# Kernel optimization log

Hardware: AMD Instinct MI355X
Metric: run time of the kernel (lower is better)

Reference implementation:

```python
import jax, jax.numpy as jnp
import numpy as np

N_EMBD = 384
N_HEADS = 6
HEAD_SIZE = N_EMBD // N_HEADS  # 64
LN_EPS = 1e-5


def _layernorm(x, g, b):
    mu = jnp.mean(x, axis=-1, keepdims=True)
    var = jnp.var(x, axis=-1, keepdims=True)
    return (x - mu) * jax.lax.rsqrt(var + LN_EPS) * g + b


def setup_inputs() -> dict:
    key = jax.random.key(0)
    ks = jax.random.split(key, 12)
    B, T, C, H, D = 128, 256, N_EMBD, N_HEADS, HEAD_SIZE
    s_in = 1.0 / np.sqrt(C)
    s_ff = 1.0 / np.sqrt(4 * C)
    return {
        "x": jax.random.normal(ks[0], (B, T, C), dtype=jnp.float32),
        "ln1_g": jnp.ones((C,), jnp.float32),
        "ln1_b": jnp.zeros((C,), jnp.float32),
        "Wq": jax.random.uniform(ks[1], (H, C, D), jnp.float32, -s_in, s_in),
        "Wk": jax.random.uniform(ks[2], (H, C, D), jnp.float32, -s_in, s_in),
        "Wv": jax.random.uniform(ks[3], (H, C, D), jnp.float32, -s_in, s_in),
        "Wo": jax.random.uniform(ks[4], (C, C), jnp.float32, -s_in, s_in),
        "bo": jnp.zeros((C,), jnp.float32),
        "ln2_g": jnp.ones((C,), jnp.float32),
        "ln2_b": jnp.zeros((C,), jnp.float32),
        "W1": jax.random.uniform(ks[5], (C, 4 * C), jnp.float32, -s_in, s_in),
        "b1": jnp.zeros((4 * C,), jnp.float32),
        "W2": jax.random.uniform(ks[6], (4 * C, C), jnp.float32, -s_ff, s_ff),
        "b2": jnp.zeros((C,), jnp.float32),
    }


def reference(x, ln1_g, ln1_b, Wq, Wk, Wv, Wo, bo, ln2_g, ln2_b, W1, b1, W2, b2):
    # Dropout layers are identity (eval mode).
    B, T, C = x.shape
    h = _layernorm(x, ln1_g, ln1_b)
    # Per-head projections: [B,T,C] x [H,C,D] -> [B,H,T,D]
    q = jnp.einsum('btc,hcd->bhtd', h, Wq)
    k = jnp.einsum('btc,hcd->bhtd', h, Wk)
    v = jnp.einsum('btc,hcd->bhtd', h, Wv)
    scale = HEAD_SIZE ** (-0.5)
    scores = jnp.einsum('bhtd,bhsd->bhts', q, k) * scale  # [B,H,T,T]
    causal = jnp.tril(jnp.ones((T, T), dtype=bool))
    scores = jnp.where(causal, scores, jnp.float32(-jnp.inf))
    wei = jax.nn.softmax(scores, axis=-1)
    attn = jnp.einsum('bhts,bhsd->bhtd', wei, v)  # [B,H,T,D]
    attn = attn.transpose(0, 2, 1, 3).reshape(B, T, C)  # concat heads
    x = x + attn @ Wo + bo
    h2 = _layernorm(x, ln2_g, ln2_b)
    ff = jax.nn.relu(h2 @ W1 + b1) @ W2 + b2
    return x + ff
```

## Files before the change

kernel.cpp:

```cpp
#include <hip/hip_runtime.h>

typedef unsigned int u32;
typedef unsigned short u16;
typedef __bf16 bf16_t;
typedef float f32x4 __attribute__((ext_vector_type(4)));
typedef bf16_t bfrag __attribute__((ext_vector_type(8)));
typedef u16 u16x8 __attribute__((ext_vector_type(8)));
typedef u16 u16x4 __attribute__((ext_vector_type(4)));

__device__ inline u16 f2bf(float f) {
    union { float f; u32 u; } v; v.f = f;
    u32 r = v.u + 0x7fffu + ((v.u >> 16) & 1u);
    return (u16)(r >> 16);
}
__device__ inline float bf2f(u16 h) {
    union { u32 u; float f; } v; v.u = ((u32)h) << 16; return v.f;
}

__device__ inline f32x4 mfma16(bfrag a, bfrag b, f32x4 c) {
    return __builtin_amdgcn_mfma_f32_16x16x32_bf16(a, b, c, 0, 0, 0);
}

__device__ inline void gload_lds16(const void* g, void* l) {
    __builtin_amdgcn_global_load_lds((const __attribute__((address_space(1))) u32*)g,
                                     (__attribute__((address_space(3))) u32*)l, 16, 0, 0);
}

__device__ inline float redmax16(float v) {
    #pragma unroll
    for (int m = 1; m < 16; m <<= 1) v = fmaxf(v, __shfl_xor(v, m));
    return v;
}
__device__ inline float redsum16(float v) {
    #pragma unroll
    for (int m = 1; m < 16; m <<= 1) v += __shfl_xor(v, m);
    return v;
}

#define NTOK 32768
#define QKV_ELEMS 12582912

__global__ __launch_bounds__(256) void prep_weights(
    const float* __restrict__ Wq, const float* __restrict__ Wk,
    const float* __restrict__ Wv, const float* __restrict__ Wo,
    const float* __restrict__ W1, const float* __restrict__ W2,
    u16* __restrict__ wqkvT, u16* __restrict__ woT,
    u16* __restrict__ w1T, u16* __restrict__ w2T)
{
    __shared__ float tile[64][65];
    const int b = blockIdx.x;
    const float* src; u16* dst;
    int sr0, sc0, srs, dr0, dc0, drs;
    if (b < 36) {
        int i = b / 6, j = b - i * 6;
        src = Wo;  srs = 384;  sr0 = i * 64; sc0 = j * 64;
        dst = woT; drs = 384;  dr0 = j * 64; dc0 = i * 64;
    } else if (b < 180) {
        int t = b - 36; int i = t / 24, j = t - i * 24;
        src = W1;  srs = 1536; sr0 = i * 64; sc0 = j * 64;
        dst = w1T; drs = 384;  dr0 = j * 64; dc0 = i * 64;
    } else if (b < 324) {
        int t = b - 180; int i = t / 6, j = t - i * 6;
        src = W2;  srs = 384;  sr0 = i * 64; sc0 = j * 64;
        dst = w2T; drs = 1536; dr0 = j * 64; dc0 = i * 64;
    } else {
        int t = b - 324;
        int m2 = t / 36; t -= m2 * 36;
        int h = t / 6, tt = t - h * 6;
        src = (m2 == 0) ? Wq : ((m2 == 1) ? Wk : Wv);
        srs = 64;  sr0 = h * 384 + tt * 64; sc0 = 0;
        dst = wqkvT; drs = 384; dr0 = m2 * 384 + h * 64; dc0 = tt * 64;
    }
    const int lane = threadIdx.x & 63, grp = threadIdx.x >> 6;
    #pragma unroll
    for (int i = 0; i < 16; i++) {
        int r = grp * 16 + i;
        tile[r][lane] = src[(size_t)(sr0 + r) * srs + sc0 + lane];
    }
    __syncthreads();
    #pragma unroll
    for (int i = 0; i < 16; i++) {
        int r = grp * 16 + i;
        dst[(size_t)(dr0 + r) * drs + dc0 + lane] = f2bf(tile[lane][r]);
    }
}

__global__ __launch_bounds__(256) void ln_f32(
    const float* __restrict__ x, const float* __restrict__ g,
    const float* __restrict__ b, u16* __restrict__ out)
{
    const int row = blockIdx.x * 4 + (threadIdx.x >> 6);
    const int lane = threadIdx.x & 63;
    const float2* xr = (const float2*)(x + (size_t)row * 384);
    float2 v[3];
    float s = 0.f, s2 = 0.f;
    #pragma unroll
    for (int i = 0; i < 3; i++) {
        v[i] = xr[lane + i * 64];
        s += v[i].x + v[i].y; s2 += v[i].x * v[i].x + v[i].y * v[i].y;
    }
    #pragma unroll
    for (int m = 1; m < 64; m <<= 1) { s += __shfl_xor(s, m); s2 += __shfl_xor(s2, m); }
    float mean = s * (1.f / 384.f);
    float rstd = rsqrtf(s2 * (1.f / 384.f) - mean * mean + 1e-5f);
    u32* op = (u32*)(out + (size_t)row * 384);
    #pragma unroll
    for (int i = 0; i < 3; i++) {
        int c = (lane + i * 64) * 2;
        u32 lo = f2bf((v[i].x - mean) * rstd * g[c] + b[c]);
        u32 hi = f2bf((v[i].y - mean) * rstd * g[c + 1] + b[c + 1]);
        op[lane + i * 64] = lo | (hi << 16);
    }
}

__global__ __launch_bounds__(256) void ln_bf16(
    const u16* __restrict__ x, const float* __restrict__ g,
    const float* __restrict__ b, u16* __restrict__ out)
{
    const int row = blockIdx.x * 4 + (threadIdx.x >> 6);
    const int lane = threadIdx.x & 63;
    const u32* xr = (const u32*)(x + (size_t)row * 384);
    float vx[3], vy[3];
    float s = 0.f, s2 = 0.f;
    #pragma unroll
    for (int i = 0; i < 3; i++) {
        u32 w = xr[lane + i * 64];
        vx[i] = bf2f((u16)(w & 0xffffu));
        vy[i] = bf2f((u16)(w >> 16));
        s += vx[i] + vy[i]; s2 += vx[i] * vx[i] + vy[i] * vy[i];
    }
    #pragma unroll
    for (int m = 1; m < 64; m <<= 1) { s += __shfl_xor(s, m); s2 += __shfl_xor(s2, m); }
    float mean = s * (1.f / 384.f);
    float rstd = rsqrtf(s2 * (1.f / 384.f) - mean * mean + 1e-5f);
    u32* op = (u32*)(out + (size_t)row * 384);
    #pragma unroll
    for (int i = 0; i < 3; i++) {
        int c = (lane + i * 64) * 2;
        u32 lo = f2bf((vx[i] - mean) * rstd * g[c] + b[c]);
        u32 hi = f2bf((vy[i] - mean) * rstd * g[c + 1] + b[c + 1]);
        op[lane + i * 64] = lo | (hi << 16);
    }
}

template<int EPI, int NT>
__global__ __launch_bounds__(256, 4) void gemm_m97(
    const u16* __restrict__ A, const u16* __restrict__ Bt,
    const float* __restrict__ bias, const void* __restrict__ resid,
    void* __restrict__ outp, int M, int N)
{
    const int K = NT * 64;
    __shared__ __align__(16) u16 smem[17408];
    u16* As = smem;
    u16* Bs = smem + 8192;
    const int tid = threadIdx.x, wave = tid >> 6, lane = tid & 63;
    const int nbn = N >> 7;
    const int nwg = gridDim.x;
    const int bid = blockIdx.x;
    const int wg = (bid & 7) * (nwg >> 3) + (bid >> 3);
    const int bm = wg / nbn, bn = wg - bm * nbn;
    const int rowA0 = bm << 7, rowB0 = bn << 7;
    const int wm = (wave >> 1) << 6, wn = (wave & 1) << 6;
    const int lr = lane >> 3, lc = lane & 7;
    f32x4 acc[4][4] = {};

    for (int t = 0; t < NT; ++t) {
        const int ko = t << 6;
        #pragma unroll
        for (int p = 0; p < 4; p++) {
            const int idx = p * 4 + wave;
            const int r = idx * 8 + lr;
            const int csrc = ((lc ^ (r & 7)) << 3);
            gload_lds16(A + (size_t)(rowA0 + r) * K + ko + csrc, &As[idx * 512]);
            gload_lds16(Bt + (size_t)(rowB0 + r) * K + ko + csrc, &Bs[idx * 512]);
        }
        __syncthreads();
        #pragma unroll
        for (int kk = 0; kk < 2; kk++) {
            bfrag af[4], bfr[4];
            #pragma unroll
            for (int mt = 0; mt < 4; mt++) {
                const int row = wm + mt * 16 + (lane & 15);
                af[mt] = *(const bfrag*)((const char*)As + row * 128 +
                          (((kk * 4 + (lane >> 4)) ^ (row & 7)) << 4));
            }
            #pragma unroll
            for (int nt = 0; nt < 4; nt++) {
                const int row = wn + nt * 16 + (lane & 15);
                bfr[nt] = *(const bfrag*)((const char*)Bs + row * 128 +
                          (((kk * 4 + (lane >> 4)) ^ (row & 7)) << 4));
            }
            #pragma unroll
            for (int mt = 0; mt < 4; mt++)
                #pragma unroll
                for (int nt = 0; nt < 4; nt++)
                    acc[mt][nt] = mfma16(af[mt], bfr[nt], acc[mt][nt]);
        }
        __syncthreads();
    }

    if constexpr (EPI != 3) {
        #pragma unroll
        for (int mt = 0; mt < 4; mt++)
            #pragma unroll
            for (int nt = 0; nt < 4; nt++)
                #pragma unroll
                for (int r2 = 0; r2 < 4; r2++) {
                    const int lr2 = wm + mt * 16 + ((lane >> 4) << 2) + r2;
                    const int lc2 = wn + nt * 16 + (lane & 15);
                    float v = acc[mt][nt][r2];
                    if constexpr (EPI == 0) { if (rowB0 + lc2 < 384) v *= 0.125f; }
                    smem[lr2 * 136 + lc2] = f2bf(v);
                }
        __syncthreads();
        #pragma unroll
        for (int it = 0; it < 8; it++) {
            const int flat = it * 2048 + tid * 8;
            const int row = flat >> 7, col = flat & 127;
            u16x8 pk = *(const u16x8*)&smem[row * 136 + col];
            const int gr = rowA0 + row;
            const int gc0 = rowB0 + col;
            if constexpr (EPI == 0) {
                const int m2 = gc0 / 384, rem = gc0 - m2 * 384;
                const int hh = rem >> 6, d0 = rem & 63;
                const int bb = gr >> 8, tt2 = gr & 255;
                *(u16x8*)&((u16*)outp)[(size_t)m2 * QKV_ELEMS +
                    ((size_t)((bb * 6 + hh) * 256 + tt2) << 6) + d0] = pk;
            } else if constexpr (EPI == 1) {
                const float* rr = (const float*)resid + (size_t)gr * N + gc0;
                float4 ra = *(const float4*)rr;
                float4 rb = *(const float4*)(rr + 4);
                float4 ba = *(const float4*)&bias[gc0];
                float4 bb4 = *(const float4*)&bias[gc0 + 4];
                u16x8 o;
                o[0] = f2bf(bf2f(pk[0]) + ra.x + ba.x);
                o[1] = f2bf(bf2f(pk[1]) + ra.y + ba.y);
                o[2] = f2bf(bf2f(pk[2]) + ra.z + ba.z);
                o[3] = f2bf(bf2f(pk[3]) + ra.w + ba.w);
                o[4] = f2bf(bf2f(pk[4]) + rb.x + bb4.x);
                o[5] = f2bf(bf2f(pk[5]) + rb.y + bb4.y);
                o[6] = f2bf(bf2f(pk[6]) + rb.z + bb4.z);
                o[7] = f2bf(bf2f(pk[7]) + rb.w + bb4.w);
                *(u16x8*)&((u16*)outp)[(size_t)gr * N + gc0] = o;
            } else {
                float4 ba = *(const float4*)&bias[gc0];
                float4 bb4 = *(const float4*)&bias[gc0 + 4];
                u16x8 o;
                float t0;
                t0 = bf2f(pk[0]) + ba.x;  o[0] = f2bf(t0 > 0.f ? t0 : 0.f);
                t0 = bf2f(pk[1]) + ba.y;  o[1] = f2bf(t0 > 0.f ? t0 : 0.f);
                t0 = bf2f(pk[2]) + ba.z;  o[2] = f2bf(t0 > 0.f ? t0 : 0.f);
                t0 = bf2f(pk[3]) + ba.w;  o[3] = f2bf(t0 > 0.f ? t0 : 0.f);
                t0 = bf2f(pk[4]) + bb4.x; o[4] = f2bf(t0 > 0.f ? t0 : 0.f);
                t0 = bf2f(pk[5]) + bb4.y; o[5] = f2bf(t0 > 0.f ? t0 : 0.f);
                t0 = bf2f(pk[6]) + bb4.z; o[6] = f2bf(t0 > 0.f ? t0 : 0.f);
                t0 = bf2f(pk[7]) + bb4.w; o[7] = f2bf(t0 > 0.f ? t0 : 0.f);
                *(u16x8*)&((u16*)outp)[(size_t)gr * N + gc0] = o;
            }
        }
    } else {
        float* sf = (float*)smem;
        #pragma unroll
        for (int half = 0; half < 2; half++) {
            if ((wm >> 6) == half) {
                #pragma unroll
                for (int mt = 0; mt < 4; mt++)
                    #pragma unroll
                    for (int nt = 0; nt < 4; nt++)
                        #pragma unroll
                        for (int r2 = 0; r2 < 4; r2++) {
                            const int lr2 = mt * 16 + ((lane >> 4) << 2) + r2;
                            const int lc2 = wn + nt * 16 + (lane & 15);
                            sf[lr2 * 132 + lc2] = acc[mt][nt][r2];
                        }
            }
            __syncthreads();
            #pragma unroll
            for (int it = 0; it < 8; it++) {
                const int flat4 = it * 1024 + tid * 4;
                const int row = flat4 >> 7, col = flat4 & 127;
                float4 v = *(const float4*)&sf[row * 132 + col];
                const int gr = rowA0 + half * 64 + row;
                const int gc0 = rowB0 + col;
                u16x4 rr = *(const u16x4*)&((const u16*)resid)[(size_t)gr * N + gc0];
                float4 b4 = *(const float4*)&bias[gc0];
                float4 o;
                o.x = v.x + bf2f(rr[0]) + b4.x;
                o.y = v.y + bf2f(rr[1]) + b4.y;
                o.z = v.z + bf2f(rr[2]) + b4.z;
                o.w = v.w + bf2f(rr[3]) + b4.w;
                *(float4*)&((float*)outp)[(size_t)gr * N + gc0] = o;
            }
            __syncthreads();
        }
    }
}

__global__ __launch_bounds__(512) void attn_kernel(
    const u16* __restrict__ q, const u16* __restrict__ k, const u16* __restrict__ v,
    u16* __restrict__ outp)
{
    __shared__ __align__(16) u16 Ks[256 * 64];
    __shared__ __align__(16) u16 Vt[64 * 256];
    __shared__ __align__(16) u16 Ps[8 * 512];
    const int bh = blockIdx.x;
    const int tid = threadIdx.x, wave = tid >> 6, lane = tid & 63;
    const u16* qb = q + (size_t)bh * 16384;
    const u16* kb = k + (size_t)bh * 16384;
    const u16* vb = v + (size_t)bh * 16384;

    #pragma unroll
    for (int p = 0; p < 4; p++) {
        const int idx = p * 8 + wave;
        const int r = idx * 8 + (lane >> 3);
        const int csrc = (((lane & 7) ^ (r & 7)) << 3);
        gload_lds16(kb + (size_t)r * 64 + csrc, &Ks[idx * 512]);
    }
    #pragma unroll
    for (int p = 0; p < 4; p++) {
        const int e = (p * 512 + tid) * 8;
        const int key = e >> 6, d0 = e & 63;
        u16x8 raw = *(const u16x8*)(vb + (size_t)key * 64 + d0);
        #pragma unroll
        for (int j = 0; j < 8; j++) {
            const int d = d0 + j;
            Vt[d * 256 + (((key >> 3) ^ (d & 7)) << 3) + (key & 7)] = raw[j];
        }
    }
    __syncthreads();

    const int bI = bh / 6, hh = bh - bI * 6;

    #pragma unroll
    for (int t = 0; t < 2; t++) {
        const int qtile = (t == 0) ? wave : (15 - wave);
        const int qrowbase = qtile * 16;
        bfrag qf[2];
        {
            const int r = qrowbase + (lane & 15);
            qf[0] = *(const bfrag*)(qb + (size_t)r * 64 + ((lane >> 4) << 3));
            qf[1] = *(const bfrag*)(qb + (size_t)r * 64 + 32 + ((lane >> 4) << 3));
        }
        f32x4 S[16];
        #pragma unroll
        for (int kt = 0; kt < 16; kt++) {
            if (kt <= qtile) {
                f32x4 s = {0.f, 0.f, 0.f, 0.f};
                const int key = kt * 16 + (lane & 15);
                const char* kbase = (const char*)Ks + key * 128;
                s = mfma16(qf[0], *(const bfrag*)(kbase + ((((lane >> 4)) ^ (key & 7)) << 4)), s);
                s = mfma16(qf[1], *(const bfrag*)(kbase + (((4 + (lane >> 4)) ^ (key & 7)) << 4)), s);
                if (kt == qtile) {
                    const int qit = (lane >> 4) << 2;
                    #pragma unroll
                    for (int r2 = 0; r2 < 4; r2++)
                        if ((lane & 15) > qit + r2) s[r2] = -1e30f;
                }
                S[kt] = s;
            }
        }
        float mx[4] = {-1e30f, -1e30f, -1e30f, -1e30f};
        #pragma unroll
        for (int kt = 0; kt < 16; kt++) if (kt <= qtile)
            #pragma unroll
            for (int r2 = 0; r2 < 4; r2++) mx[r2] = fmaxf(mx[r2], S[kt][r2]);
        #pragma unroll
        for (int r2 = 0; r2 < 4; r2++) mx[r2] = redmax16(mx[r2]);
        float sm[4] = {0.f, 0.f, 0.f, 0.f};
        #pragma unroll
        for (int kt = 0; kt < 16; kt++) if (kt <= qtile)
            #pragma unroll
            for (int r2 = 0; r2 < 4; r2++) {
                float p = __expf(S[kt][r2] - mx[r2]);
                S[kt][r2] = p; sm[r2] += p;
            }
        #pragma unroll
        for (int r2 = 0; r2 < 4; r2++) sm[r2] = redsum16(sm[r2]);

        f32x4 O[4] = {};
        u16* Pw = &Ps[wave * 512];
        const int nch = (qtile + 2) >> 1;
        #pragma unroll
        for (int ch = 0; ch < 8; ch++) {
            if (ch < nch) {
                #pragma unroll
                for (int ktl = 0; ktl < 2; ktl++) {
                    const int kt = ch * 2 + ktl;
                    const int keyl = ktl * 16 + (lane & 15);
                    const int cidx = keyl >> 3;
                    #pragma unroll
                    for (int r2 = 0; r2 < 4; r2++) {
                        const int qq = ((lane >> 4) << 2) + r2;
                        float pv = (kt <= qtile) ? S[kt][r2] : 0.f;
                        Pw[qq * 32 + ((cidx ^ (qq & 3)) << 3) + (keyl & 7)] = f2bf(pv);
                    }
                }
                const int qq = lane & 15;
                bfrag pa = *(const bfrag*)(Pw + qq * 32 + (((lane >> 4) ^ (qq & 3)) << 3));
                #pragma unroll
                for (int dt = 0; dt < 4; dt++) {
                    const int d = dt * 16 + (lane & 15);
                    const int cc = ch * 4 + (lane >> 4);
                    bfrag vf = *(const bfrag*)((const char*)Vt + d * 512 + ((cc ^ (d & 7)) << 4));
                    O[dt] = mfma16(pa, vf, O[dt]);
                }
            }
        }
        #pragma unroll
        for (int dt = 0; dt < 4; dt++) {
            #pragma unroll
            for (int r2 = 0; r2 < 4; r2++) {
                const int qg = qrowbase + ((lane >> 4) << 2) + r2;
                const float val = O[dt][r2] / sm[r2];
                outp[(size_t)(bI * 256 + qg) * 384 + hh * 64 + dt * 16 + (lane & 15)] = f2bf(val);
            }
        }
    }
}

extern "C" void kernel_launch(void* const* d_in, const int* in_sizes, int n_in,
                              void* d_out, int out_size, void* d_ws, size_t ws_size,
                              hipStream_t stream)
{
    const float* x    = (const float*)d_in[0];
    const float* ln1g = (const float*)d_in[1];
    const float* ln1b = (const float*)d_in[2];
    const float* Wq   = (const float*)d_in[3];
    const float* Wk   = (const float*)d_in[4];
    const float* Wv   = (const float*)d_in[5];
    const float* Wo   = (const float*)d_in[6];
    const float* bo   = (const float*)d_in[7];
    const float* ln2g = (const float*)d_in[8];
    const float* ln2b = (const float*)d_in[9];
    const float* W1   = (const float*)d_in[10];
    const float* b1   = (const float*)d_in[11];
    const float* W2   = (const float*)d_in[12];
    const float* b2   = (const float*)d_in[13];

    if (ws_size < 230031360u) return;

    char* ws = (char*)d_ws;
    u16*   wqkvT = (u16*)(ws + 0);
    u16*   woT   = (u16*)(ws + 884736);
    u16*   w1T   = (u16*)(ws + 1179648);
    u16*   w2T   = (u16*)(ws + 2359296);
    u16*   hbuf  = (u16*)(ws + 3538944);
    u16*   qbuf  = (u16*)(ws + 28704768);
    u16*   kbuf  = (u16*)(ws + 53870592);
    u16*   vbuf  = (u16*)(ws + 79036416);
    u16*   x2h   = (u16*)(ws + 104202240);
    u16*   mid   = (u16*)(ws + 129368064);
    float* out   = (float*)d_out;

    prep_weights<<<432, 256, 0, stream>>>(Wq, Wk, Wv, Wo, W1, W2, wqkvT, woT, w1T, w2T);
    ln_f32<<<8192, 256, 0, stream>>>(x, ln1g, ln1b, hbuf);
    gemm_m97<0, 6><<<2304, 256, 0, stream>>>(hbuf, wqkvT, nullptr, nullptr, qbuf,
                                             NTOK, 1152);
    attn_kernel<<<768, 512, 0, stream>>>(qbuf, kbuf, vbuf, hbuf);
    gemm_m97<1, 6><<<768, 256, 0, stream>>>(hbuf, woT, bo, x, x2h, NTOK, 384);
    ln_bf16<<<8192, 256, 0, stream>>>(x2h, ln2g, ln2b, qbuf);
    gemm_m97<2, 6><<<3072, 256, 0, stream>>>(qbuf, w1T, b1, nullptr, mid, NTOK, 1536);
    gemm_m97<3, 24><<<768, 256, 0, stream>>>(mid, w2T, b2, x2h, out, NTOK, 384);
}
```

Measured before the change: 234.5 us.

## Enlarge GEMM tiles to 256x128 with 512-thread workgroups

The GEMM kernel now uses 8 waves per workgroup and a 256-row by 128-column output tile, so each loaded B tile is reused across twice as many A rows. Grid sizes are halved, and the staged epilogue writes in two or four passes through LDS. The cost is more LDS per block (48KB) and fewer workgroups, which can reduce occupancy or leave CUs idle on the smaller N=384 GEMMs.

```diff
diff --git a/kernel.cpp b/kernel.cpp
--- a/kernel.cpp
+++ b/kernel.cpp
@@ -144,22 +144,22 @@
 }
 
 template<int EPI, int NT>
-__global__ __launch_bounds__(256, 4) void gemm_m97(
+__global__ __launch_bounds__(512, 4) void gemm_big(
     const u16* __restrict__ A, const u16* __restrict__ Bt,
     const float* __restrict__ bias, const void* __restrict__ resid,
     void* __restrict__ outp, int M, int N)
 {
     const int K = NT * 64;
-    __shared__ __align__(16) u16 smem[17408];
+    __shared__ __align__(16) u16 smem[24576];
     u16* As = smem;
-    u16* Bs = smem + 8192;
+    u16* Bs = smem + 16384;
     const int tid = threadIdx.x, wave = tid >> 6, lane = tid & 63;
     const int nbn = N >> 7;
     const int nwg = gridDim.x;
     const int bid = blockIdx.x;
     const int wg = (bid & 7) * (nwg >> 3) + (bid >> 3);
     const int bm = wg / nbn, bn = wg - bm * nbn;
-    const int rowA0 = bm << 7, rowB0 = bn << 7;
+    const int rowA0 = bm << 8, rowB0 = bn << 7;
     const int wm = (wave >> 1) << 6, wn = (wave & 1) << 6;
     const int lr = lane >> 3, lc = lane & 7;
     f32x4 acc[4][4] = {};
@@ -167,12 +167,18 @@
     for (int t = 0; t < NT; ++t) {
         const int ko = t << 6;
         #pragma unroll
-        for (int p = 0; p < 4; p++) {
-            const int idx = p * 4 + wave;
-            const int r = idx * 8 + lr;
-            const int csrc = ((lc ^ (r & 7)) << 3);
-            gload_lds16(A + (size_t)(rowA0 + r) * K + ko + csrc, &As[idx * 512]);
-            gload_lds16(Bt + (size_t)(rowB0 + r) * K + ko + csrc, &Bs[idx * 512]);
+        for (int p = 0; p < 6; p++) {
+            const int idx = p * 8 + wave;
+            if (idx < 32) {
+                const int r = idx * 8 + lr;
+                gload_lds16(A + (size_t)(rowA0 + r) * K + ko + ((lc ^ (r & 7)) << 3),
+                            &As[idx * 512]);
+            } else {
+                const int c = idx - 32;
+                const int r = c * 8 + lr;
+                gload_lds16(Bt + (size_t)(rowB0 + r) * K + ko + ((lc ^ (r & 7)) << 3),
+                            &Bs[c * 512]);
+            }
         }
         __syncthreads();
         #pragma unroll
@@ -201,68 +207,74 @@
 
     if constexpr (EPI != 3) {
         #pragma unroll
-        for (int mt = 0; mt < 4; mt++)
-            #pragma unroll
-            for (int nt = 0; nt < 4; nt++)
+        for (int h = 0; h < 2; h++) {
+            if ((wm >> 7) == h) {
                 #pragma unroll
-                for (int r2 = 0; r2 < 4; r2++) {
-                    const int lr2 = wm + mt * 16 + ((lane >> 4) << 2) + r2;
-                    const int lc2 = wn + nt * 16 + (lane & 15);
-                    float v = acc[mt][nt][r2];
-                    if constexpr (EPI == 0) { if (rowB0 + lc2 < 384) v *= 0.125f; }
-                    smem[lr2 * 136 + lc2] = f2bf(v);
+                for (int mt = 0; mt < 4; mt++)
+                    #pragma unroll
+                    for (int nt = 0; nt < 4; nt++)
+                        #pragma unroll
+                        for (int r2 = 0; r2 < 4; r2++) {
+                            const int lr2 = (wm & 127) + mt * 16 + ((lane >> 4) << 2) + r2;
+                            const int lc2 = wn + nt * 16 + (lane & 15);
+                            float v = acc[mt][nt][r2];
+                            if constexpr (EPI == 0) { if (rowB0 + lc2 < 384) v *= 0.125f; }
+                            smem[lr2 * 136 + lc2] = f2bf(v);
+                        }
+            }
+            __syncthreads();
+            #pragma unroll
+            for (int it = 0; it < 4; it++) {
+                const int flat = (it * 512 + tid) * 8;
+                const int row = flat >> 7, col = flat & 127;
+                u16x8 pk = *(const u16x8*)&smem[row * 136 + col];
+                const int gr = rowA0 + h * 128 + row;
+                const int gc0 = rowB0 + col;
+                if constexpr (EPI == 0) {
+                    const int m2 = gc0 / 384, rem = gc0 - m2 * 384;
+                    const int hh = rem >> 6, d0 = rem & 63;
+                    const int bb = gr >> 8, tt2 = gr & 255;
+                    *(u16x8*)&((u16*)outp)[(size_t)m2 * QKV_ELEMS +
+                        ((size_t)((bb * 6 + hh) * 256 + tt2) << 6) + d0] = pk;
+                } else if constexpr (EPI == 1) {
+                    const float* rr = (const float*)resid + (size_t)gr * N + gc0;
+                    float4 ra = *(const float4*)rr;
+                    float4 rb = *(const float4*)(rr + 4);
+                    float4 ba = *(const float4*)&bias[gc0];
+                    float4 bb4 = *(const float4*)&bias[gc0 + 4];
+                    u16x8 o;
+                    o[0] = f2bf(bf2f(pk[0]) + ra.x + ba.x);
+                    o[1] = f2bf(bf2f(pk[1]) + ra.y + ba.y);
+                    o[2] = f2bf(bf2f(pk[2]) + ra.z + ba.z);
+                    o[3] = f2bf(bf2f(pk[3]) + ra.w + ba.w);
+                    o[4] = f2bf(bf2f(pk[4]) + rb.x + bb4.x);
+                    o[5] = f2bf(bf2f(pk[5]) + rb.y + bb4.y);
+                    o[6] = f2bf(bf2f(pk[6]) + rb.z + bb4.z);
+                    o[7] = f2bf(bf2f(pk[7]) + rb.w + bb4.w);
+                    *(u16x8*)&((u16*)outp)[(size_t)gr * N + gc0] = o;
+                } else {
+                    float4 ba = *(const float4*)&bias[gc0];
+                    float4 bb4 = *(const float4*)&bias[gc0 + 4];
+                    u16x8 o;
+                    float t0;
+                    t0 = bf2f(pk[0]) + ba.x;  o[0] = f2bf(t0 > 0.f ? t0 : 0.f);
+                    t0 = bf2f(pk[1]) + ba.y;  o[1] = f2bf(t0 > 0.f ? t0 : 0.f);
+                    t0 = bf2f(pk[2]) + ba.z;  o[2] = f2bf(t0 > 0.f ? t0 : 0.f);
+                    t0 = bf2f(pk[3]) + ba.w;  o[3] = f2bf(t0 > 0.f ? t0 : 0.f);
+                    t0 = bf2f(pk[4]) + bb4.x; o[4] = f2bf(t0 > 0.f ? t0 : 0.f);
+                    t0 = bf2f(pk[5]) + bb4.y; o[5] = f2bf(t0 > 0.f ? t0 : 0.f);
+                    t0 = bf2f(pk[6]) + bb4.z; o[6] = f2bf(t0 > 0.f ? t0 : 0.f);
+                    t0 = bf2f(pk[7]) + bb4.w; o[7] = f2bf(t0 > 0.f ? t0 : 0.f);
+                    *(u16x8*)&((u16*)outp)[(size_t)gr * N + gc0] = o;
                 }
-        __syncthreads();
-        #pragma unroll
-        for (int it = 0; it < 8; it++) {
-            const int flat = it * 2048 + tid * 8;
-            const int row = flat >> 7, col = flat & 127;
-            u16x8 pk = *(const u16x8*)&smem[row * 136 + col];
-            const int gr = rowA0 + row;
-            const int gc0 = rowB0 + col;
-            if constexpr (EPI == 0) {
-                const int m2 = gc0 / 384, rem = gc0 - m2 * 384;
-                const int hh = rem >> 6, d0 = rem & 63;
-                const int bb = gr >> 8, tt2 = gr & 255;
-                *(u16x8*)&((u16*)outp)[(size_t)m2 * QKV_ELEMS +
-                    ((size_t)((bb * 6 + hh) * 256 + tt2) << 6) + d0] = pk;
-            } else if constexpr (EPI == 1) {
-                const float* rr = (const float*)resid + (size_t)gr * N + gc0;
-                float4 ra = *(const float4*)rr;
-                float4 rb = *(const float4*)(rr + 4);
-                float4 ba = *(const float4*)&bias[gc0];
-                float4 bb4 = *(const float4*)&bias[gc0 + 4];
-                u16x8 o;
-                o[0] = f2bf(bf2f(pk[0]) + ra.x + ba.x);
-                o[1] = f2bf(bf2f(pk[1]) + ra.y + ba.y);
-                o[2] = f2bf(bf2f(pk[2]) + ra.z + ba.z);
-                o[3] = f2bf(bf2f(pk[3]) + ra.w + ba.w);
-                o[4] = f2bf(bf2f(pk[4]) + rb.x + bb4.x);
-                o[5] = f2bf(bf2f(pk[5]) + rb.y + bb4.y);
-                o[6] = f2bf(bf2f(pk[6]) + rb.z + bb4.z);
-                o[7] = f2bf(bf2f(pk[7]) + rb.w + bb4.w);
-                *(u16x8*)&((u16*)outp)[(size_t)gr * N + gc0] = o;
-            } else {
-                float4 ba = *(const float4*)&bias[gc0];
-                float4 bb4 = *(const float4*)&bias[gc0 + 4];
-                u16x8 o;
-                float t0;
-                t0 = bf2f(pk[0]) + ba.x;  o[0] = f2bf(t0 > 0.f ? t0 : 0.f);
-                t0 = bf2f(pk[1]) + ba.y;  o[1] = f2bf(t0 > 0.f ? t0 : 0.f);
-                t0 = bf2f(pk[2]) + ba.z;  o[2] = f2bf(t0 > 0.f ? t0 : 0.f);
-                t0 = bf2f(pk[3]) + ba.w;  o[3] = f2bf(t0 > 0.f ? t0 : 0.f);
-                t0 = bf2f(pk[4]) + bb4.x; o[4] = f2bf(t0 > 0.f ? t0 : 0.f);
-                t0 = bf2f(pk[5]) + bb4.y; o[5] = f2bf(t0 > 0.f ? t0 : 0.f);
-                t0 = bf2f(pk[6]) + bb4.z; o[6] = f2bf(t0 > 0.f ? t0 : 0.f);
-                t0 = bf2f(pk[7]) + bb4.w; o[7] = f2bf(t0 > 0.f ? t0 : 0.f);
-                *(u16x8*)&((u16*)outp)[(size_t)gr * N + gc0] = o;
-            }
+            }
+            __syncthreads();
         }
     } else {
         float* sf = (float*)smem;
         #pragma unroll
-        for (int half = 0; half < 2; half++) {
-            if ((wm >> 6) == half) {
+        for (int q = 0; q < 4; q++) {
+            if ((wm >> 6) == q) {
                 #pragma unroll
                 for (int mt = 0; mt < 4; mt++)
                     #pragma unroll
@@ -276,11 +288,11 @@
             }
             __syncthreads();
             #pragma unroll
-            for (int it = 0; it < 8; it++) {
-                const int flat4 = it * 1024 + tid * 4;
-                const int row = flat4 >> 7, col = flat4 & 127;
+            for (int it = 0; it < 4; it++) {
+                const int e4 = (it * 512 + tid) * 4;
+                const int row = e4 >> 7, col = e4 & 127;
                 float4 v = *(const float4*)&sf[row * 132 + col];
-                const int gr = rowA0 + half * 64 + row;
+                const int gr = rowA0 + q * 64 + row;
                 const int gc0 = rowB0 + col;
                 u16x4 rr = *(const u16x4*)&((const u16*)resid)[(size_t)gr * N + gc0];
                 float4 b4 = *(const float4*)&bias[gc0];
@@ -454,11 +466,11 @@
 
     prep_weights<<<432, 256, 0, stream>>>(Wq, Wk, Wv, Wo, W1, W2, wqkvT, woT, w1T, w2T);
     ln_f32<<<8192, 256, 0, stream>>>(x, ln1g, ln1b, hbuf);
-    gemm_m97<0, 6><<<2304, 256, 0, stream>>>(hbuf, wqkvT, nullptr, nullptr, qbuf,
+    gemm_big<0, 6><<<1152, 512, 0, stream>>>(hbuf, wqkvT, nullptr, nullptr, qbuf,
                                              NTOK, 1152);
     attn_kernel<<<768, 512, 0, stream>>>(qbuf, kbuf, vbuf, hbuf);
-    gemm_m97<1, 6><<<768, 256, 0, stream>>>(hbuf, woT, bo, x, x2h, NTOK, 384);
+    gemm_big<1, 6><<<384, 512, 0, stream>>>(hbuf, woT, bo, x, x2h, NTOK, 384);
     ln_bf16<<<8192, 256, 0, stream>>>(x2h, ln2g, ln2b, qbuf);
-    gemm_m97<2, 6><<<3072, 256, 0, stream>>>(qbuf, w1T, b1, nullptr, mid, NTOK, 1536);
-    gemm_m97<3, 24><<<768, 256, 0, stream>>>(mid, w2T, b2, x2h, out, NTOK, 384);
-}
+    gemm_big<2, 6><<<1536, 512, 0, stream>>>(qbuf, w1T, b1, nullptr, mid, NTOK, 1536);
+    gemm_big<3, 24><<<384, 512, 0, stream>>>(mid, w2T, b2, x2h, out, NTOK, 384);
+}
```

Measured after the change: 261.4 us. 1.11x slower.
